# Kernel optimization log

Hardware: AMD Instinct MI355X
Metric: run time of the kernel (lower is better)

Reference implementation:

```python
import jax, jax.numpy as jnp
import numpy as np

B, T, C = 4, 4096, 1024


def setup_inputs() -> dict:
    key = jax.random.key(0)
    k_x, k_f, k_g, k_p = jax.random.split(key, 4)
    scale = 1.0 / np.sqrt(C)  # keep gate pre-activations well-scaled
    return {
        "x": jax.random.normal(k_x, (B, T, C), dtype=jnp.float32),
        "W_f_x": jax.random.normal(k_f, (C, C), dtype=jnp.float32) * scale,
        "W_g_x": jax.random.normal(k_g, (C, C), dtype=jnp.float32) * scale,
        "W_proj": jax.random.normal(k_p, (C, C), dtype=jnp.float32) * scale,
    }


def _cfc_scan(a, b):
    """Solve h_t = a_t * h_{t-1} + b_t with h_{-1}=0 along axis 1 (T).

    Associative op on linear maps: (A_l,B_l) then (A_r,B_r) composes to
    (A_r*A_l, A_r*B_l + B_r). With h_init=0, h_t = B-component.
    """
    def op(l, r):
        al, bl = l
        ar, br = r
        return ar * al, ar * bl + br
    _, h = jax.lax.associative_scan(op, (a, b), axis=1)
    return h


def reference(x, W_f_x, W_g_x, W_proj):
    # Gates depend on x only (parallel mode). nn.Linear: x @ W.T
    f = jax.nn.sigmoid(jnp.einsum("btc,dc->btd", x, W_f_x))  # (B,T,C)
    g = jnp.tanh(jnp.einsum("btc,dc->btd", x, W_g_x))        # (B,T,C)
    h = _cfc_scan(f, (1.0 - f) * g)                           # (B,T,C)
    return jnp.einsum("btc,dc->btd", h, W_proj)               # c_proj
```

## Files before the change

kernel.cpp:

```cpp
#include <hip/hip_runtime.h>
#include <hip/hip_bf16.h>
#include <stdint.h>

#define TT 4096
#define BB 4
#define CC 1024
#define MM (BB * TT)
#define NCHUNK 64
#define CHUNK_T (TT / NCHUNK)
#define NCHAIN (BB * CC)

typedef float f32x4 __attribute__((ext_vector_type(4)));
typedef __bf16 bf16x8 __attribute__((ext_vector_type(8)));

__device__ __forceinline__ float b2f(ushort u) {
  union { float f; uint32_t v; } x; x.v = ((uint32_t)u) << 16; return x.f;
}
__device__ __forceinline__ ushort f2b(float f) {
  union { float f; uint32_t u; } x; x.f = f;
  uint32_t r = x.u + 0x7fffu + ((x.u >> 16) & 1u);
  return (ushort)(r >> 16);
}

__device__ __forceinline__ void async_copy16(const ushort* g, ushort* l) {
  __builtin_amdgcn_global_load_lds(
      (__attribute__((address_space(1))) void*)(g),
      (__attribute__((address_space(3))) void*)(l), 16, 0, 0);
}

__global__ __launch_bounds__(256) void cvt_all(const float* __restrict__ x,
                                               const float* __restrict__ wf,
                                               const float* __restrict__ wg,
                                               const float* __restrict__ wp,
                                               ushort* __restrict__ xb,
                                               ushort* __restrict__ wcat,
                                               ushort* __restrict__ wpb) {
  const int i = blockIdx.x * 256 + threadIdx.x;
  const float* s; ushort* d; int off;
  if (i < 4194304)            { s = x;  d = xb;              off = i; }
  else if (i < 4456448)       { s = wf; d = wcat;            off = i - 4194304; }
  else if (i < 4718592)       { s = wg; d = wcat + 1048576;  off = i - 4456448; }
  else                        { s = wp; d = wpb;             off = i - 4718592; }
  float4 v = ((const float4*)s)[off];
  ushort4 o;
  o.x = f2b(v.x); o.y = f2b(v.y); o.z = f2b(v.z); o.w = f2b(v.w);
  ((ushort4*)d)[off] = o;
}

template <int MODE>
__global__ __launch_bounds__(256) void gemm_bt(const ushort* __restrict__ A,
                                               const ushort* __restrict__ Bw,
                                               float* __restrict__ outF,
                                               ushort* __restrict__ outB, int N) {
  constexpr int K = CC;
  __shared__ __align__(16) ushort sA[128 * 64];
  __shared__ __align__(16) ushort sB[128 * 64];
  const int tid = threadIdx.x;
  const int lane = tid & 63;
  const int wid = tid >> 6;
  const int wm = wid >> 1, wn = wid & 1;
  const long m0 = (long)blockIdx.y * 128;
  const long n0 = (long)blockIdx.x * 128;

  f32x4 acc[4][4];
#pragma unroll
  for (int i = 0; i < 4; ++i)
#pragma unroll
    for (int j = 0; j < 4; ++j) acc[i][j] = (f32x4){0.f, 0.f, 0.f, 0.f};

  const int srow8 = lane >> 3;
  const int g8 = (lane & 7) ^ (srow8 & 7);
  const ushort* Ab = A + (m0 + srow8) * K + g8 * 8;
  const ushort* Bb = Bw + (n0 + srow8) * K + g8 * 8;
  const int kq = lane >> 4;
  const int rlo = lane & 15;
  const int rx = rlo & 7;

  for (int k0 = 0; k0 < K; k0 += 64) {
#pragma unroll
    for (int ch = wid; ch < 32; ch += 4) {
      if (ch < 16)
        async_copy16(Ab + (long)(ch * 8) * K + k0, &sA[ch * 512 + lane * 8]);
      else
        async_copy16(Bb + (long)((ch - 16) * 8) * K + k0, &sB[(ch - 16) * 512 + lane * 8]);
    }
    __syncthreads();

#pragma unroll
    for (int s = 0; s < 2; ++s) {
      const int slot = (s * 4 + kq) ^ rx;
      bf16x8 af[4], bfr[4];
#pragma unroll
      for (int i = 0; i < 4; ++i) {
        af[i]  = *(const bf16x8*)&sA[(wm * 64 + i * 16 + rlo) * 64 + slot * 8];
        bfr[i] = *(const bf16x8*)&sB[(wn * 64 + i * 16 + rlo) * 64 + slot * 8];
      }
#pragma unroll
      for (int i = 0; i < 4; ++i)
#pragma unroll
        for (int j = 0; j < 4; ++j)
          acc[i][j] = __builtin_amdgcn_mfma_f32_16x16x32_bf16(bfr[j], af[i], acc[i][j], 0, 0, 0);
    }
    __syncthreads();
  }

  const int mloc = lane & 15;
  const int rq = lane >> 4;
#pragma unroll
  for (int i = 0; i < 4; ++i) {
    const long m = m0 + wm * 64 + i * 16 + mloc;
#pragma unroll
    for (int j = 0; j < 4; ++j) {
      const long nb = n0 + wn * 64 + j * 16 + rq * 4;
      const f32x4 v = acc[i][j];
      if (MODE == 0) {
        *(f32x4*)(outF + m * N + nb) = v;
      } else {
        float act[4];
        if (n0 < CC) {
#pragma unroll
          for (int r = 0; r < 4; ++r)
            act[r] = __builtin_amdgcn_rcpf(1.f + __expf(-v[r]));
        } else {
#pragma unroll
          for (int r = 0; r < 4; ++r)
            act[r] = fmaf(-2.f, __builtin_amdgcn_rcpf(1.f + __expf(2.f * v[r])), 1.f);
        }
        ushort4 o;
        o.x = f2b(act[0]); o.y = f2b(act[1]); o.z = f2b(act[2]); o.w = f2b(act[3]);
        *(ushort4*)(outB + m * (long)N + nb) = o;
      }
    }
  }
}

__global__ __launch_bounds__(256) void scan_pass1(const ushort* __restrict__ P,
                                                  float* __restrict__ cA,
                                                  float* __restrict__ cB) {
  const int pc = blockIdx.x * 256 + threadIdx.x;
  const int chunk = blockIdx.y;
  const int b = pc >> 8, c4 = (pc & 255) * 4;
  const ushort4* p =
      (const ushort4*)(P + (size_t)(b * TT + chunk * CHUNK_T) * (2 * CC) + c4);
  float A[4] = {1.f, 1.f, 1.f, 1.f};
  float h[4] = {0.f, 0.f, 0.f, 0.f};
#pragma unroll 4
  for (int i = 0; i < CHUNK_T; ++i) {
    const ushort4 fu = p[0];
    const ushort4 gu = p[CC / 4];
    p += 2 * CC / 4;
    const float f[4] = {b2f(fu.x), b2f(fu.y), b2f(fu.z), b2f(fu.w)};
    const float g[4] = {b2f(gu.x), b2f(gu.y), b2f(gu.z), b2f(gu.w)};
#pragma unroll
    for (int r = 0; r < 4; ++r) {
      A[r] *= f[r];
      h[r] = fmaf(f[r], h[r], (1.f - f[r]) * g[r]);
    }
  }
  const int ci = chunk * NCHAIN + b * CC + c4;
  *(f32x4*)(cA + ci) = (f32x4){A[0], A[1], A[2], A[3]};
  *(f32x4*)(cB + ci) = (f32x4){h[0], h[1], h[2], h[3]};
}

__global__ __launch_bounds__(256) void scan_pass2(const float* __restrict__ cA,
                                                  const float* __restrict__ cB,
                                                  float* __restrict__ hinit) {
  const int chain = blockIdx.x * 256 + threadIdx.x;
  float h = 0.f;
  for (int j = 0; j < NCHUNK; ++j) {
    hinit[j * NCHAIN + chain] = h;
    h = fmaf(cA[j * NCHAIN + chain], h, cB[j * NCHAIN + chain]);
  }
}

__global__ __launch_bounds__(256) void scan_pass3(const ushort* __restrict__ P,
                                                  const float* __restrict__ hinit,
                                                  ushort* __restrict__ H) {
  const int pc = blockIdx.x * 256 + threadIdx.x;
  const int chunk = blockIdx.y;
  const int b = pc >> 8, c4 = (pc & 255) * 4;
  f32x4 hv = *(const f32x4*)(hinit + chunk * NCHAIN + b * CC + c4);
  float h[4] = {hv[0], hv[1], hv[2], hv[3]};
  const ushort4* p =
      (const ushort4*)(P + (size_t)(b * TT + chunk * CHUNK_T) * (2 * CC) + c4);
  ushort4* hp = (ushort4*)(H + (size_t)(b * TT + chunk * CHUNK_T) * CC + c4);
#pragma unroll 4
  for (int i = 0; i < CHUNK_T; ++i) {
    const ushort4 fu = p[0];
    const ushort4 gu = p[CC / 4];
    p += 2 * CC / 4;
    const float f[4] = {b2f(fu.x), b2f(fu.y), b2f(fu.z), b2f(fu.w)};
    const float g[4] = {b2f(gu.x), b2f(gu.y), b2f(gu.z), b2f(gu.w)};
    ushort4 o;
#pragma unroll
    for (int r = 0; r < 4; ++r)
      h[r] = fmaf(f[r], h[r], (1.f - f[r]) * g[r]);
    o.x = f2b(h[0]); o.y = f2b(h[1]); o.z = f2b(h[2]); o.w = f2b(h[3]);
    *hp = o;
    hp += CC / 4;
  }
}

extern "C" void kernel_launch(void* const* d_in, const int* in_sizes, int n_in,
                              void* d_out, int out_size, void* d_ws, size_t ws_size,
                              hipStream_t stream) {
  const float* x  = (const float*)d_in[0];
  const float* Wf = (const float*)d_in[1];
  const float* Wg = (const float*)d_in[2];
  const float* Wp = (const float*)d_in[3];

  char* ws = (char*)d_ws;
  ushort* xb   = (ushort*)(ws);
  ushort* Hb   = xb;
  ushort* Wcat = (ushort*)(ws + 33554432);
  ushort* Wpb  = (ushort*)(ws + 33554432 + 4194304);
  ushort* P    = (ushort*)(ws + 33554432 + 4194304 + 2097152);
  char* tail   = ws + 33554432 + 4194304 + 2097152 + 67108864;
  float* cA    = (float*)(tail);
  float* cB    = (float*)(tail + 1048576);
  float* hinit = (float*)(tail + 2097152);
  (void)ws_size; (void)in_sizes; (void)n_in; (void)out_size;

  cvt_all<<<19456, 256, 0, stream>>>(x, Wf, Wg, Wp, xb, Wcat, Wpb);

  dim3 g1(2 * CC / 128, MM / 128);
  gemm_bt<1><<<g1, 256, 0, stream>>>(xb, Wcat, nullptr, P, 2 * CC);

  dim3 gs(NCHAIN / 4 / 256, NCHUNK);
  scan_pass1<<<gs, 256, 0, stream>>>(P, cA, cB);
  scan_pass2<<<NCHAIN / 256, 256, 0, stream>>>(cA, cB, hinit);
  scan_pass3<<<gs, 256, 0, stream>>>(P, hinit, Hb);

  dim3 g3(CC / 128, MM / 128);
  gemm_bt<0><<<g3, 256, 0, stream>>>(Hb, Wpb, (float*)d_out, nullptr, CC);
}
```

Baseline: 297.6 us.

## Rewrite GEMM with 256x256 tiles, 4-stage async LDS pipeline and XCD swizzle

Restructures both GEMMs to use 512-thread blocks computing 256x256 output tiles with K-steps of 32. Global-to-LDS async copies run through a 4-buffer ring with two stages in flight, using vmcnt waits and raw barriers in place of full syncthreads. Block IDs are remapped so that neighbouring tiles land on the same XCD, and MFMA sections raise wave priority. The aim is to hide load latency, raise arithmetic intensity and improve L2 locality. The cost is higher register and LDS pressure, plus a hard-coded K loop count.

After: 278.4 us. 1.07x faster.

```diff
diff --git a/kernel.cpp b/kernel.cpp
--- a/kernel.cpp
+++ b/kernel.cpp
@@ -48,70 +48,113 @@
 }
 
 template <int MODE>
-__global__ __launch_bounds__(256) void gemm_bt(const ushort* __restrict__ A,
-                                               const ushort* __restrict__ Bw,
-                                               float* __restrict__ outF,
-                                               ushort* __restrict__ outB, int N) {
+__global__ __launch_bounds__(512, 2) void gemm_bt(const ushort* __restrict__ A,
+                                                  const ushort* __restrict__ Bw,
+                                                  float* __restrict__ outF,
+                                                  ushort* __restrict__ outB, int N) {
   constexpr int K = CC;
-  __shared__ __align__(16) ushort sA[128 * 64];
-  __shared__ __align__(16) ushort sB[128 * 64];
+  __shared__ __align__(16) ushort sA[4 * 256 * 32];
+  __shared__ __align__(16) ushort sB[4 * 256 * 32];
+
   const int tid = threadIdx.x;
   const int lane = tid & 63;
-  const int wid = tid >> 6;
-  const int wm = wid >> 1, wn = wid & 1;
-  const long m0 = (long)blockIdx.y * 128;
-  const long n0 = (long)blockIdx.x * 128;
-
-  f32x4 acc[4][4];
-#pragma unroll
-  for (int i = 0; i < 4; ++i)
+  const int w = tid >> 6;
+  const int wm = w >> 2;
+  const int wn = w & 3;
+
+  const int nbx = N >> 8;
+  const int cpx = (int)gridDim.x >> 3;
+  const int bid = blockIdx.x;
+  const int wg = (bid & 7) * cpx + (bid >> 3);
+  const long n0 = (long)(wg % nbx) << 8;
+  const long m0 = (long)(wg / nbx) << 8;
+
+  const int srow = lane >> 2;
+  const int goct = (lane & 3) ^ ((lane >> 3) & 3);
+  const ushort* gA0 = A + (m0 + w * 16 + srow) * K + goct * 8;
+  const ushort* gB0 = Bw + (n0 + w * 16 + srow) * K + goct * 8;
+  const ushort* gA1 = gA0 + 128 * (long)K;
+  const ushort* gB1 = gB0 + 128 * (long)K;
+  ushort* dA0 = &sA[w * 512 + lane * 8];
+  ushort* dA1 = dA0 + 4096;
+  ushort* dB0 = &sB[w * 512 + lane * 8];
+  ushort* dB1 = dB0 + 4096;
+
+  const int rlo = lane & 15;
+  const int kq = lane >> 4;
+  const int slot = kq ^ ((rlo >> 1) & 3);
+  const ushort* rA = &sA[wm * 4096 + rlo * 32 + slot * 8];
+  const ushort* rB = &sB[wn * 2048 + rlo * 32 + slot * 8];
+
+  f32x4 acc[8][4];
+#pragma unroll
+  for (int i = 0; i < 8; ++i)
 #pragma unroll
     for (int j = 0; j < 4; ++j) acc[i][j] = (f32x4){0.f, 0.f, 0.f, 0.f};
 
-  const int srow8 = lane >> 3;
-  const int g8 = (lane & 7) ^ (srow8 & 7);
-  const ushort* Ab = A + (m0 + srow8) * K + g8 * 8;
-  const ushort* Bb = Bw + (n0 + srow8) * K + g8 * 8;
-  const int kq = lane >> 4;
-  const int rlo = lane & 15;
-  const int rx = rlo & 7;
-
-  for (int k0 = 0; k0 < K; k0 += 64) {
-#pragma unroll
-    for (int ch = wid; ch < 32; ch += 4) {
-      if (ch < 16)
-        async_copy16(Ab + (long)(ch * 8) * K + k0, &sA[ch * 512 + lane * 8]);
-      else
-        async_copy16(Bb + (long)((ch - 16) * 8) * K + k0, &sB[(ch - 16) * 512 + lane * 8]);
+  auto stage = [&](int buf, int ts) {
+    const int o = ts * 32;
+    const int lo = buf * 8192;
+    async_copy16(gA0 + o, dA0 + lo);
+    async_copy16(gA1 + o, dA1 + lo);
+    async_copy16(gB0 + o, dB0 + lo);
+    async_copy16(gB1 + o, dB1 + lo);
+  };
+
+  auto body = [&](int buf, bool do_stage, int ts) {
+    bf16x8 af[8], bfr[4];
+    const int lo = buf * 8192;
+#pragma unroll
+    for (int i = 0; i < 8; ++i) af[i] = *(const bf16x8*)(rA + lo + i * 512);
+#pragma unroll
+    for (int j = 0; j < 4; ++j) bfr[j] = *(const bf16x8*)(rB + lo + j * 512);
+    if (do_stage) stage((buf + 2) & 3, ts);
+    __builtin_amdgcn_s_setprio(1);
+#pragma unroll
+    for (int i = 0; i < 8; ++i)
+#pragma unroll
+      for (int j = 0; j < 4; ++j)
+        acc[i][j] = __builtin_amdgcn_mfma_f32_16x16x32_bf16(bfr[j], af[i], acc[i][j], 0, 0, 0);
+    __builtin_amdgcn_s_setprio(0);
+  };
+
+  stage(0, 0);
+  stage(1, 1);
+  asm volatile("s_waitcnt vmcnt(4)" ::: "memory");
+  __builtin_amdgcn_s_barrier();
+  __builtin_amdgcn_sched_barrier(0);
+
+  for (int t4 = 0; t4 < 7; ++t4) {
+#pragma unroll
+    for (int u = 0; u < 4; ++u) {
+      body(u, true, t4 * 4 + u + 2);
+      asm volatile("s_waitcnt vmcnt(4)" ::: "memory");
+      __builtin_amdgcn_s_barrier();
+      __builtin_amdgcn_sched_barrier(0);
     }
-    __syncthreads();
-
-#pragma unroll
-    for (int s = 0; s < 2; ++s) {
-      const int slot = (s * 4 + kq) ^ rx;
-      bf16x8 af[4], bfr[4];
-#pragma unroll
-      for (int i = 0; i < 4; ++i) {
-        af[i]  = *(const bf16x8*)&sA[(wm * 64 + i * 16 + rlo) * 64 + slot * 8];
-        bfr[i] = *(const bf16x8*)&sB[(wn * 64 + i * 16 + rlo) * 64 + slot * 8];
-      }
-#pragma unroll
-      for (int i = 0; i < 4; ++i)
-#pragma unroll
-        for (int j = 0; j < 4; ++j)
-          acc[i][j] = __builtin_amdgcn_mfma_f32_16x16x32_bf16(bfr[j], af[i], acc[i][j], 0, 0, 0);
-    }
-    __syncthreads();
-  }
+  }
+  body(0, true, 30);
+  asm volatile("s_waitcnt vmcnt(4)" ::: "memory");
+  __builtin_amdgcn_s_barrier();
+  __builtin_amdgcn_sched_barrier(0);
+  body(1, true, 31);
+  asm volatile("s_waitcnt vmcnt(4)" ::: "memory");
+  __builtin_amdgcn_s_barrier();
+  __builtin_amdgcn_sched_barrier(0);
+  body(2, false, 0);
+  asm volatile("s_waitcnt vmcnt(0)" ::: "memory");
+  __builtin_amdgcn_s_barrier();
+  __builtin_amdgcn_sched_barrier(0);
+  body(3, false, 0);
 
   const int mloc = lane & 15;
-  const int rq = lane >> 4;
-#pragma unroll
-  for (int i = 0; i < 4; ++i) {
-    const long m = m0 + wm * 64 + i * 16 + mloc;
+  const int nq = (lane >> 4) * 4;
+#pragma unroll
+  for (int i = 0; i < 8; ++i) {
+    const long m = m0 + wm * 128 + i * 16 + mloc;
 #pragma unroll
     for (int j = 0; j < 4; ++j) {
-      const long nb = n0 + wn * 64 + j * 16 + rq * 4;
+      const long nb = n0 + wn * 64 + j * 16 + nq;
       const f32x4 v = acc[i][j];
       if (MODE == 0) {
         *(f32x4*)(outF + m * N + nb) = v;
@@ -223,14 +266,12 @@
 
   cvt_all<<<19456, 256, 0, stream>>>(x, Wf, Wg, Wp, xb, Wcat, Wpb);
 
-  dim3 g1(2 * CC / 128, MM / 128);
-  gemm_bt<1><<<g1, 256, 0, stream>>>(xb, Wcat, nullptr, P, 2 * CC);
+  gemm_bt<1><<<512, 512, 0, stream>>>(xb, Wcat, nullptr, P, 2 * CC);
 
   dim3 gs(NCHAIN / 4 / 256, NCHUNK);
   scan_pass1<<<gs, 256, 0, stream>>>(P, cA, cB);
   scan_pass2<<<NCHAIN / 256, 256, 0, stream>>>(cA, cB, hinit);
   scan_pass3<<<gs, 256, 0, stream>>>(P, hinit, Hb);
 
-  dim3 g3(CC / 128, MM / 128);
-  gemm_bt<0><<<g3, 256, 0, stream>>>(Hb, Wpb, (float*)d_out, nullptr, CC);
-}
+  gemm_bt<0><<<256, 512, 0, stream>>>(Hb, Wpb, (float*)d_out, nullptr, CC);
+}
```
